# Performance work log

Measured on AMD Instinct MI355X. Metric: run time of the kernel, lower is better.

## Reference

```python
import jax, jax.numpy as jnp
import numpy as np

EPS = 1e-5

def conv3x3(x, w, b, stride=1):
    y = jax.lax.conv_general_dilated(x, w, (stride, stride), ((1, 1), (1, 1)),
                                     dimension_numbers=('NCHW', 'OIHW', 'NCHW'))
    return y + b[None, :, None, None]

def batchnorm(x, gamma, beta):
    # training-mode BN (PyTorch default): biased batch statistics over N,H,W
    mean = x.mean((0, 2, 3), keepdims=True)
    var = ((x - mean) ** 2).mean((0, 2, 3), keepdims=True)
    return (x - mean) * jax.lax.rsqrt(var + EPS) * gamma[None, :, None, None] + beta[None, :, None, None]

def deform_conv3x3(x, offset, w, b):
    # torchvision DeformConv2d: kernel 3x3, stride 1, pad 1, deform_groups=1
    B, C, H, W = x.shape
    K = 3
    off = offset.reshape(B, K * K, 2, H, W)  # per kernel tap: (dy, dx)
    ky, kx = jnp.meshgrid(jnp.arange(K) - 1, jnp.arange(K) - 1, indexing='ij')
    ky = ky.reshape(-1).astype(x.dtype)  # [9]
    kx = kx.reshape(-1).astype(x.dtype)
    y0 = jnp.arange(H, dtype=x.dtype)[:, None]
    x0 = jnp.arange(W, dtype=x.dtype)[None, :]
    py = y0[None, None] + ky[None, :, None, None] + off[:, :, 0]  # [B,9,H,W]
    px = x0[None, None] + kx[None, :, None, None] + off[:, :, 1]
    y_lo = jnp.floor(py)
    x_lo = jnp.floor(px)
    ly = (py - y_lo)[:, None]  # [B,1,9,H,W]
    lx = (px - x_lo)[:, None]
    xf = x.reshape(B, C, H * W)

    def gather(iy, ix):
        valid = ((iy >= 0) & (iy < H) & (ix >= 0) & (ix < W)).astype(x.dtype)
        iyc = jnp.clip(iy, 0, H - 1).astype(jnp.int32)
        ixc = jnp.clip(ix, 0, W - 1).astype(jnp.int32)
        idx = iyc * W + ixc  # [B,9,H,W]
        g = jax.vmap(lambda xb, ib: xb[:, ib.reshape(-1)].reshape(C, K * K, H, W))(xf, idx)
        return g * valid[:, None]  # zero padding outside -> [B,C,9,H,W]

    v00 = gather(y_lo, x_lo)
    v01 = gather(y_lo, x_lo + 1)
    v10 = gather(y_lo + 1, x_lo)
    v11 = gather(y_lo + 1, x_lo + 1)
    sampled = (v00 * (1 - ly) * (1 - lx) + v01 * (1 - ly) * lx
               + v10 * ly * (1 - lx) + v11 * ly * lx)  # [B,C,9,H,W]
    out = jnp.einsum('bckhw,ock->bohw', sampled, w.reshape(w.shape[0], C, K * K))
    return out + b[None, :, None, None]


def setup_inputs() -> dict:
    key = jax.random.key(0)
    ks = jax.random.split(key, 8)
    B, C, H, W = 4, 128, 64, 64
    x = jax.random.normal(ks[0], (B, C, H, W), jnp.float32)
    w_off = jax.random.normal(ks[1], (18, C, 3, 3), jnp.float32) * 0.01  # small offsets
    b_off = jnp.zeros((18,), jnp.float32)
    w_d = jax.random.normal(ks[2], (C, C, 3, 3), jnp.float32) * 0.03
    b_d = jnp.zeros((C,), jnp.float32)
    w1 = jax.random.normal(ks[3], (C, C, 3, 3), jnp.float32) * 0.03
    b1 = jnp.zeros((C,), jnp.float32)
    g1 = jnp.ones((C,), jnp.float32)
    beta1 = jnp.zeros((C,), jnp.float32)
    w2 = jax.random.normal(ks[4], (C, C, 3, 3), jnp.float32) * 0.03
    b2 = jnp.zeros((C,), jnp.float32)
    g2 = jnp.ones((C,), jnp.float32)
    beta2 = jnp.zeros((C,), jnp.float32)
    return {"x": x, "w_off": w_off, "b_off": b_off, "w_d": w_d, "b_d": b_d,
            "w1": w1, "b1": b1, "g1": g1, "beta1": beta1,
            "w2": w2, "b2": b2, "g2": g2, "beta2": beta2}


def reference(x, w_off, b_off, w_d, b_d, w1, b1, g1, beta1, w2, b2, g2, beta2):
    offset = conv3x3(x, w_off, b_off)
    d_out = deform_conv3x3(x, offset, w_d, b_d)
    out = jax.nn.relu(batchnorm(conv3x3(x, w1, b1), g1, beta1))
    out = batchnorm(conv3x3(out, w2, b2), g2, beta2)
    return jax.nn.relu(d_out + out)
```

## Files before the change

kernel.cpp:

```cpp
#include <hip/hip_runtime.h>

#define HH 64
#define WW 64
#define CC 128
#define HWSZ 4096

typedef __attribute__((ext_vector_type(8))) short short8v;
typedef __attribute__((ext_vector_type(4))) short short4v;
typedef __attribute__((ext_vector_type(4))) float floatx4;

__device__ __forceinline__ unsigned short f2bf(float f) {
    unsigned u = __float_as_uint(f);
    return (unsigned short)((u + 0x7FFFu + ((u >> 16) & 1u)) >> 16);
}
__device__ __forceinline__ float bf2f(unsigned short h) {
    return __uint_as_float(((unsigned)h) << 16);
}

__global__ void prepack_k(const float* __restrict__ w, unsigned short* __restrict__ blob,
                          int oc_total, int OCP)
{
    int i = blockIdx.x * 256 + threadIdx.x;
    if (i >= 36 * OCP * 32) return;
    int kr = i & 31;
    int rest = i >> 5;
    int oc = rest % OCP;
    int kc = rest / OCP;
    int k = kc * 32 + kr;
    float v = 0.f;
    if (oc < oc_total) v = w[((size_t)oc * CC + k / 9) * 9 + (k % 9)];
    unsigned short h = f2bf(v);
    unsigned short l = f2bf(v - bf2f(h));
    size_t base = (size_t)(kc * 2) * OCP * 40;
    blob[base + (size_t)oc * 40 + kr] = h;
    blob[base + (size_t)(OCP + oc) * 40 + kr] = l;
}

template<int TAG, int OCP, int MFR, int NFR, int WM, bool BN_IN, bool STATS>
__global__ __launch_bounds__(256)
void gemm_k(const float* __restrict__ in, const float* __restrict__ blobf,
            const float* __restrict__ bias,
            const float* __restrict__ bnscale, const float* __restrict__ bnshift,
            float* __restrict__ out, float* __restrict__ ssum, float* __restrict__ ssq,
            int oc_total)
{
    __shared__ __align__(16) unsigned short Al[2][64][40];
    __shared__ __align__(16) unsigned short Bl[2][OCP][40];
    const int tid = threadIdx.x;
    const int lane = tid & 63;
    const int wid = tid >> 6;
    const int b = blockIdx.x >> 6;
    const int y = blockIdx.x & 63;
    const int wm = wid % WM;
    const int wn = wid / WM;
    const int m0 = wm * MFR * 16;
    const int n0 = wn * NFR * 16;
    const int lrow = lane & 15;
    const int lkg  = (lane >> 4) * 8;

    floatx4 acc[MFR][NFR];
#pragma unroll
    for (int mi = 0; mi < MFR; ++mi)
#pragma unroll
        for (int nj = 0; nj < NFR; ++nj)
            acc[mi][nj] = {0.f, 0.f, 0.f, 0.f};

    const unsigned short* blb = (const unsigned short*)blobf;
    const float* inb = in + (size_t)b * CC * HWSZ;
    const int px = tid & 63;
    const int kr0 = (tid >> 6) * 8;

    for (int kc = 0; kc < 36; ++kc) {
        __syncthreads();
        short8v vh, vl;
#pragma unroll
        for (int j = 0; j < 8; ++j) {
            int k = kc * 32 + kr0 + j;
            int ic = k / 9;
            int kk = k - ic * 9;
            int ky = kk / 3;
            int gy = y + ky - 1;
            int gx = px + (kk - ky * 3) - 1;
            float v = 0.f;
            if ((unsigned)gy < (unsigned)HH && (unsigned)gx < (unsigned)WW) {
                v = inb[(size_t)ic * HWSZ + gy * WW + gx];
                if (BN_IN) v = fmaxf(fmaf(v, bnscale[ic], bnshift[ic]), 0.f);
            }
            unsigned short h = f2bf(v);
            vh[j] = (short)h;
            vl[j] = (short)f2bf(v - bf2f(h));
        }
        *(short8v*)&Al[0][px][kr0] = vh;
        *(short8v*)&Al[1][px][kr0] = vl;
        {
            const float4* src = (const float4*)(blb + (size_t)(kc * 2) * OCP * 40);
            float4* dst = (float4*)&Bl[0][0][0];
            const int n16 = (2 * OCP * 40) / 8;
            for (int i = tid; i < n16; i += 256) dst[i] = src[i];
        }
        __syncthreads();
        short8v af[2][MFR], bfr[2][NFR];
#pragma unroll
        for (int mi = 0; mi < MFR; ++mi) {
            af[0][mi] = *(const short8v*)&Al[0][m0 + mi * 16 + lrow][lkg];
            af[1][mi] = *(const short8v*)&Al[1][m0 + mi * 16 + lrow][lkg];
        }
#pragma unroll
        for (int nj = 0; nj < NFR; ++nj) {
            bfr[0][nj] = *(const short8v*)&Bl[0][n0 + nj * 16 + lrow][lkg];
            bfr[1][nj] = *(const short8v*)&Bl[1][n0 + nj * 16 + lrow][lkg];
        }
#pragma unroll
        for (int mi = 0; mi < MFR; ++mi)
#pragma unroll
            for (int nj = 0; nj < NFR; ++nj) {
                acc[mi][nj] = __builtin_amdgcn_mfma_f32_16x16x32_bf16(af[0][mi], bfr[0][nj], acc[mi][nj], 0, 0, 0);
                acc[mi][nj] = __builtin_amdgcn_mfma_f32_16x16x32_bf16(af[0][mi], bfr[1][nj], acc[mi][nj], 0, 0, 0);
                acc[mi][nj] = __builtin_amdgcn_mfma_f32_16x16x32_bf16(af[1][mi], bfr[0][nj], acc[mi][nj], 0, 0, 0);
            }
    }
#pragma unroll
    for (int nj = 0; nj < NFR; ++nj) {
        int oc = n0 + nj * 16 + lrow;
        float bv = (oc < oc_total) ? bias[oc] : 0.f;
        float s = 0.f, q = 0.f;
#pragma unroll
        for (int mi = 0; mi < MFR; ++mi) {
            floatx4 r = acc[mi][nj];
            r.x += bv; r.y += bv; r.z += bv; r.w += bv;
            if (oc < oc_total) {
                int pxq = m0 + mi * 16 + (lane >> 4) * 4;
                *(float4*)(out + ((size_t)b * oc_total + oc) * HWSZ + y * WW + pxq) =
                    make_float4(r.x, r.y, r.z, r.w);
            }
            if (STATS) {
                s += r.x + r.y + r.z + r.w;
                q += r.x * r.x + r.y * r.y + r.z * r.z + r.w * r.w;
            }
        }
        if (STATS) {
            s += __shfl_xor(s, 16); q += __shfl_xor(q, 16);
            s += __shfl_xor(s, 32); q += __shfl_xor(q, 32);
            if (lane < 16) { atomicAdd(&ssum[oc], s); atomicAdd(&ssq[oc], q); }
        }
    }
}

__global__ __launch_bounds__(512)
void dgemm_k(const float* __restrict__ x, const float* __restrict__ off,
             const float* __restrict__ blobf, const float* __restrict__ bd,
             float* __restrict__ dout)
{
    __shared__ __align__(16) unsigned short Al[2][64][40];
    __shared__ __align__(16) unsigned short Bl[2][CC][40];
    __shared__ __align__(16) float tw[9][64][4];
    __shared__ __align__(16) int   ti[9][64][4];
    const int tid = threadIdx.x;
    const int lane = tid & 63;
    const int wid = tid >> 6;
    const int b = blockIdx.x >> 6;
    const int y = blockIdx.x & 63;
    const int wm = wid & 1;
    const int wn = wid >> 1;
    const int m0 = wm * 32;
    const int n0 = wn * 32;
    const int lrow = lane & 15;
    const int lkg  = (lane >> 4) * 8;

    for (int e = tid; e < 9 * 64; e += 512) {
        int kk = e >> 6, px = e & 63;
        const float* ob = off + (size_t)b * 18 * HWSZ + y * WW + px;
        float dyv = ob[(2 * kk + 0) * HWSZ];
        float dxv = ob[(2 * kk + 1) * HWSZ];
        float fy = (float)(y + kk / 3 - 1) + dyv;
        float fx = (float)(px + kk % 3 - 1) + dxv;
        float yl = floorf(fy), xl = floorf(fx);
        float ly = fy - yl, lx = fx - xl;
        int iy0 = (int)yl, ix0 = (int)xl;
        int iy1 = iy0 + 1, ix1 = ix0 + 1;
        float vy0 = (iy0 >= 0 && iy0 < HH) ? 1.f : 0.f;
        float vy1 = (iy1 >= 0 && iy1 < HH) ? 1.f : 0.f;
        float vx0 = (ix0 >= 0 && ix0 < WW) ? 1.f : 0.f;
        float vx1 = (ix1 >= 0 && ix1 < WW) ? 1.f : 0.f;
        int iy0c = min(max(iy0, 0), HH - 1), iy1c = min(max(iy1, 0), HH - 1);
        int ix0c = min(max(ix0, 0), WW - 1), ix1c = min(max(ix1, 0), WW - 1);
        ti[kk][px][0] = iy0c * WW + ix0c;
        ti[kk][px][1] = iy0c * WW + ix1c;
        ti[kk][px][2] = iy1c * WW + ix0c;
        ti[kk][px][3] = iy1c * WW + ix1c;
        tw[kk][px][0] = (1.f - ly) * (1.f - lx) * vy0 * vx0;
        tw[kk][px][1] = (1.f - ly) * lx         * vy0 * vx1;
        tw[kk][px][2] = ly * (1.f - lx) * vy1 * vx0;
        tw[kk][px][3] = ly * lx         * vy1 * vx1;
    }

    floatx4 acc[2][2];
#pragma unroll
    for (int mi = 0; mi < 2; ++mi)
#pragma unroll
        for (int nj = 0; nj < 2; ++nj)
            acc[mi][nj] = {0.f, 0.f, 0.f, 0.f};

    const unsigned short* blb = (const unsigned short*)blobf;
    const float* xb = x + (size_t)b * CC * HWSZ;
    const int px = tid & 63;
    const int kr0 = (tid >> 6) * 4;

    for (int kc = 0; kc < 36; ++kc) {
        __syncthreads();
        short4v vh, vl;
#pragma unroll
        for (int j = 0; j < 4; ++j) {
            int k = kc * 32 + kr0 + j;
            int ic = k / 9;
            int kk = k - ic * 9;
            const float* xc = xb + (size_t)ic * HWSZ;
            float4 w4 = *(const float4*)&tw[kk][px][0];
            int4   i4 = *(const int4*)&ti[kk][px][0];
            float v =      w4.x * xc[i4.x];
            v = fmaf(w4.y, xc[i4.y], v);
            v = fmaf(w4.z, xc[i4.z], v);
            v = fmaf(w4.w, xc[i4.w], v);
            unsigned short h = f2bf(v);
            vh[j] = (short)h;
            vl[j] = (short)f2bf(v - bf2f(h));
        }
        *(short4v*)&Al[0][px][kr0] = vh;
        *(short4v*)&Al[1][px][kr0] = vl;
        {
            const float4* src = (const float4*)(blb + (size_t)(kc * 2) * CC * 40);
            float4* dst = (float4*)&Bl[0][0][0];
            const int n16 = (2 * CC * 40) / 8;
            for (int i = tid; i < n16; i += 512) dst[i] = src[i];
        }
        __syncthreads();
        short8v af[2][2], bfr[2][2];
#pragma unroll
        for (int mi = 0; mi < 2; ++mi) {
            af[0][mi] = *(const short8v*)&Al[0][m0 + mi * 16 + lrow][lkg];
            af[1][mi] = *(const short8v*)&Al[1][m0 + mi * 16 + lrow][lkg];
        }
#pragma unroll
        for (int nj = 0; nj < 2; ++nj) {
            bfr[0][nj] = *(const short8v*)&Bl[0][n0 + nj * 16 + lrow][lkg];
            bfr[1][nj] = *(const short8v*)&Bl[1][n0 + nj * 16 + lrow][lkg];
        }
#pragma unroll
        for (int mi = 0; mi < 2; ++mi)
#pragma unroll
            for (int nj = 0; nj < 2; ++nj) {
                acc[mi][nj] = __builtin_amdgcn_mfma_f32_16x16x32_bf16(af[0][mi], bfr[0][nj], acc[mi][nj], 0, 0, 0);
                acc[mi][nj] = __builtin_amdgcn_mfma_f32_16x16x32_bf16(af[0][mi], bfr[1][nj], acc[mi][nj], 0, 0, 0);
                acc[mi][nj] = __builtin_amdgcn_mfma_f32_16x16x32_bf16(af[1][mi], bfr[0][nj], acc[mi][nj], 0, 0, 0);
            }
    }
#pragma unroll
    for (int nj = 0; nj < 2; ++nj) {
        int oc = n0 + nj * 16 + lrow;
        float bv = bd[oc];
#pragma unroll
        for (int mi = 0; mi < 2; ++mi) {
            floatx4 r = acc[mi][nj];
            int pxq = m0 + mi * 16 + (lane >> 4) * 4;
            *(float4*)(dout + ((size_t)b * CC + oc) * HWSZ + y * WW + pxq) =
                make_float4(r.x + bv, r.y + bv, r.z + bv, r.w + bv);
        }
    }
}

__global__ void bnstat_k(const float* __restrict__ ssum, const float* __restrict__ ssq,
                         const float* __restrict__ g, const float* __restrict__ bet,
                         float* __restrict__ scale, float* __restrict__ shift)
{
    int c = threadIdx.x;
    const float invn = 1.f / (4.f * HWSZ);
    float mean = ssum[c] * invn;
    float var  = ssq[c] * invn - mean * mean;
    float sc = g[c] * rsqrtf(var + 1e-5f);
    scale[c] = sc;
    shift[c] = fmaf(-mean, sc, bet[c]);
}

__global__ __launch_bounds__(256)
void final_k(const float* __restrict__ dout, const float* __restrict__ y2,
             const float* __restrict__ scale, const float* __restrict__ shift,
             float* __restrict__ out)
{
    int i = blockIdx.x * 256 + threadIdx.x;
    int c = (i >> 10) & 127;
    float4 d = reinterpret_cast<const float4*>(dout)[i];
    float4 yv = reinterpret_cast<const float4*>(y2)[i];
    float sc = scale[c], sh = shift[c];
    float4 r;
    r.x = fmaxf(d.x + fmaf(yv.x, sc, sh), 0.f);
    r.y = fmaxf(d.y + fmaf(yv.y, sc, sh), 0.f);
    r.z = fmaxf(d.z + fmaf(yv.z, sc, sh), 0.f);
    r.w = fmaxf(d.w + fmaf(yv.w, sc, sh), 0.f);
    reinterpret_cast<float4*>(out)[i] = r;
}

extern "C" void kernel_launch(void* const* d_in, const int* in_sizes, int n_in,
                              void* d_out, int out_size, void* d_ws, size_t ws_size,
                              hipStream_t stream)
{
    const float* x     = (const float*)d_in[0];
    const float* w_off = (const float*)d_in[1];
    const float* b_off = (const float*)d_in[2];
    const float* w_d   = (const float*)d_in[3];
    const float* b_d   = (const float*)d_in[4];
    const float* w1    = (const float*)d_in[5];
    const float* b1    = (const float*)d_in[6];
    const float* g1    = (const float*)d_in[7];
    const float* be1   = (const float*)d_in[8];
    const float* w2    = (const float*)d_in[9];
    const float* b2    = (const float*)d_in[10];
    const float* g2    = (const float*)d_in[11];
    const float* be2   = (const float*)d_in[12];

    float* ws      = (float*)d_ws;
    float* off_buf = ws;
    float* y1      = off_buf + 294912;
    float* y2      = y1 + 2097152;
    float* dob     = y2 + 2097152;
    float* wo_blob = dob + 2097152;
    float* w1_blob = wo_blob + 46080;
    float* w2_blob = w1_blob + 184320;
    float* wd_blob = w2_blob + 184320;
    float* st      = wd_blob + 184320;

    hipMemsetAsync(st, 0, 512 * sizeof(float), stream);

    prepack_k<<<(36 * 32 * 32 + 255) / 256, 256, 0, stream>>>(w_off, (unsigned short*)wo_blob, 18, 32);
    prepack_k<<<(36 * 128 * 32 + 255) / 256, 256, 0, stream>>>(w1, (unsigned short*)w1_blob, 128, 128);
    prepack_k<<<(36 * 128 * 32 + 255) / 256, 256, 0, stream>>>(w2, (unsigned short*)w2_blob, 128, 128);
    prepack_k<<<(36 * 128 * 32 + 255) / 256, 256, 0, stream>>>(w_d, (unsigned short*)wd_blob, 128, 128);

    gemm_k<0, 32, 1, 2, 4, false, false><<<256, 256, 0, stream>>>(
        x, wo_blob, b_off, nullptr, nullptr, off_buf, nullptr, nullptr, 18);

    dgemm_k<<<256, 512, 0, stream>>>(x, off_buf, wd_blob, b_d, dob);

    gemm_k<1, 128, 2, 4, 2, false, true><<<256, 256, 0, stream>>>(
        x, w1_blob, b1, nullptr, nullptr, y1, st, st + 128, 128);
    bnstat_k<<<1, 128, 0, stream>>>(st, st + 128, g1, be1, st + 512, st + 640);

    gemm_k<2, 128, 2, 4, 2, true, true><<<256, 256, 0, stream>>>(
        y1, w2_blob, b2, st + 512, st + 640, y2, st + 256, st + 384, 128);
    bnstat_k<<<1, 128, 0, stream>>>(st + 256, st + 384, g2, be2, st + 768, st + 896);

    final_k<<<dim3(2048), 256, 0, stream>>>(dob, y2, st + 768, st + 896, (float*)d_out);
}
```

Baseline: 453.4 us.

## Double-buffer LDS tiles with register prefetch in conv GEMMs; use 512 threads

The conv GEMM kernels and the deformable GEMM now use two LDS buffers. The next K-chunk's global loads (input gather and weight blob) are issued into registers before the MFMAs on the current chunk, then written to the other buffer afterwards. This removes one barrier per iteration and is meant to hide global-load latency behind the matrix math. The two 128-channel conv GEMMs also move from 256 to 512 threads per block with smaller per-wave tiles. The costs are doubled LDS use and extra prefetch registers, which may lower occupancy.

```diff
diff --git a/kernel.cpp b/kernel.cpp
--- a/kernel.cpp
+++ b/kernel.cpp
@@ -36,16 +36,19 @@
     blob[base + (size_t)(OCP + oc) * 40 + kr] = l;
 }
 
-template<int TAG, int OCP, int MFR, int NFR, int WM, bool BN_IN, bool STATS>
-__global__ __launch_bounds__(256)
+template<int TAG, int OCP, int THREADS, int WM, int MFR, int NFR, bool BN_IN, bool STATS>
+__global__ __launch_bounds__(THREADS)
 void gemm_k(const float* __restrict__ in, const float* __restrict__ blobf,
             const float* __restrict__ bias,
             const float* __restrict__ bnscale, const float* __restrict__ bnshift,
             float* __restrict__ out, float* __restrict__ ssum, float* __restrict__ ssq,
             int oc_total)
 {
-    __shared__ __align__(16) unsigned short Al[2][64][40];
-    __shared__ __align__(16) unsigned short Bl[2][OCP][40];
+    constexpr int KPT   = 2048 / THREADS;
+    constexpr int NB4   = OCP * 10;
+    constexpr int NITER = (NB4 + THREADS - 1) / THREADS;
+    __shared__ __align__(16) unsigned short Al[2][2][64][40];
+    __shared__ __align__(16) unsigned short Bl[2][2][OCP][40];
     const int tid = threadIdx.x;
     const int lane = tid & 63;
     const int wid = tid >> 6;
@@ -68,47 +71,83 @@
     const unsigned short* blb = (const unsigned short*)blobf;
     const float* inb = in + (size_t)b * CC * HWSZ;
     const int px = tid & 63;
-    const int kr0 = (tid >> 6) * 8;
-
-    for (int kc = 0; kc < 36; ++kc) {
-        __syncthreads();
-        short8v vh, vl;
-#pragma unroll
-        for (int j = 0; j < 8; ++j) {
+    const int kr0 = (tid >> 6) * KPT;
+
+    float  aval[KPT], asc[KPT], ash[KPT];
+    float4 breg[NITER];
+
+    auto load_stage = [&](int kc) {
+#pragma unroll
+        for (int j = 0; j < KPT; ++j) {
             int k = kc * 32 + kr0 + j;
             int ic = k / 9;
             int kk = k - ic * 9;
             int ky = kk / 3;
             int gy = y + ky - 1;
             int gx = px + (kk - ky * 3) - 1;
-            float v = 0.f;
-            if ((unsigned)gy < (unsigned)HH && (unsigned)gx < (unsigned)WW) {
-                v = inb[(size_t)ic * HWSZ + gy * WW + gx];
-                if (BN_IN) v = fmaxf(fmaf(v, bnscale[ic], bnshift[ic]), 0.f);
-            }
-            unsigned short h = f2bf(v);
-            vh[j] = (short)h;
-            vl[j] = (short)f2bf(v - bf2f(h));
-        }
-        *(short8v*)&Al[0][px][kr0] = vh;
-        *(short8v*)&Al[1][px][kr0] = vl;
-        {
-            const float4* src = (const float4*)(blb + (size_t)(kc * 2) * OCP * 40);
-            float4* dst = (float4*)&Bl[0][0][0];
-            const int n16 = (2 * OCP * 40) / 8;
-            for (int i = tid; i < n16; i += 256) dst[i] = src[i];
-        }
-        __syncthreads();
+            aval[j] = ((unsigned)gy < (unsigned)HH && (unsigned)gx < (unsigned)WW)
+                      ? inb[(size_t)ic * HWSZ + gy * WW + gx] : 0.f;
+            if (BN_IN) { asc[j] = bnscale[ic]; ash[j] = bnshift[ic]; }
+        }
+        const float4* src = (const float4*)(blb + (size_t)(kc * 2) * OCP * 40);
+#pragma unroll
+        for (int t = 0; t < NITER; ++t) {
+            int idx = tid + t * THREADS;
+            if (idx < NB4) breg[t] = src[idx];
+        }
+    };
+    auto write_stage = [&](int buf) {
+        if constexpr (KPT == 4) {
+            short4v vh, vl;
+#pragma unroll
+            for (int j = 0; j < 4; ++j) {
+                float v = aval[j];
+                if (BN_IN) v = fmaxf(fmaf(v, asc[j], ash[j]), 0.f);
+                unsigned short h = f2bf(v);
+                vh[j] = (short)h;
+                vl[j] = (short)f2bf(v - bf2f(h));
+            }
+            *(short4v*)&Al[buf][0][px][kr0] = vh;
+            *(short4v*)&Al[buf][1][px][kr0] = vl;
+        } else {
+            short8v vh, vl;
+#pragma unroll
+            for (int j = 0; j < 8; ++j) {
+                float v = aval[j];
+                if (BN_IN) v = fmaxf(fmaf(v, asc[j], ash[j]), 0.f);
+                unsigned short h = f2bf(v);
+                vh[j] = (short)h;
+                vl[j] = (short)f2bf(v - bf2f(h));
+            }
+            *(short8v*)&Al[buf][0][px][kr0] = vh;
+            *(short8v*)&Al[buf][1][px][kr0] = vl;
+        }
+        float4* dst = (float4*)&Bl[buf][0][0][0];
+#pragma unroll
+        for (int t = 0; t < NITER; ++t) {
+            int idx = tid + t * THREADS;
+            if (idx < NB4) dst[idx] = breg[t];
+        }
+    };
+
+    load_stage(0);
+    write_stage(0);
+    __syncthreads();
+
+    for (int kc = 0; kc < 36; ++kc) {
+        const int cur = kc & 1;
+        if (kc < 35) load_stage(kc + 1);
+
         short8v af[2][MFR], bfr[2][NFR];
 #pragma unroll
         for (int mi = 0; mi < MFR; ++mi) {
-            af[0][mi] = *(const short8v*)&Al[0][m0 + mi * 16 + lrow][lkg];
-            af[1][mi] = *(const short8v*)&Al[1][m0 + mi * 16 + lrow][lkg];
+            af[0][mi] = *(const short8v*)&Al[cur][0][m0 + mi * 16 + lrow][lkg];
+            af[1][mi] = *(const short8v*)&Al[cur][1][m0 + mi * 16 + lrow][lkg];
         }
 #pragma unroll
         for (int nj = 0; nj < NFR; ++nj) {
-            bfr[0][nj] = *(const short8v*)&Bl[0][n0 + nj * 16 + lrow][lkg];
-            bfr[1][nj] = *(const short8v*)&Bl[1][n0 + nj * 16 + lrow][lkg];
+            bfr[0][nj] = *(const short8v*)&Bl[cur][0][n0 + nj * 16 + lrow][lkg];
+            bfr[1][nj] = *(const short8v*)&Bl[cur][1][n0 + nj * 16 + lrow][lkg];
         }
 #pragma unroll
         for (int mi = 0; mi < MFR; ++mi)
@@ -118,7 +157,11 @@
                 acc[mi][nj] = __builtin_amdgcn_mfma_f32_16x16x32_bf16(af[0][mi], bfr[1][nj], acc[mi][nj], 0, 0, 0);
                 acc[mi][nj] = __builtin_amdgcn_mfma_f32_16x16x32_bf16(af[1][mi], bfr[0][nj], acc[mi][nj], 0, 0, 0);
             }
+
+        if (kc < 35) write_stage(cur ^ 1);
+        __syncthreads();
     }
+
 #pragma unroll
     for (int nj = 0; nj < NFR; ++nj) {
         int oc = n0 + nj * 16 + lrow;
@@ -151,8 +194,9 @@
              const float* __restrict__ blobf, const float* __restrict__ bd,
              float* __restrict__ dout)
 {
-    __shared__ __align__(16) unsigned short Al[2][64][40];
-    __shared__ __align__(16) unsigned short Bl[2][CC][40];
+    constexpr int NITER = 3;
+    __shared__ __align__(16) unsigned short Al[2][2][64][40];
+    __shared__ __align__(16) unsigned short Bl[2][2][CC][40];
     __shared__ __align__(16) float tw[9][64][4];
     __shared__ __align__(16) int   ti[9][64][4];
     const int tid = threadIdx.x;
@@ -206,44 +250,74 @@
     const int px = tid & 63;
     const int kr0 = (tid >> 6) * 4;
 
-    for (int kc = 0; kc < 36; ++kc) {
-        __syncthreads();
-        short4v vh, vl;
+    float  g4[4][4];
+    float4 breg[NITER];
+
+    auto load_stage = [&](int kc) {
 #pragma unroll
         for (int j = 0; j < 4; ++j) {
             int k = kc * 32 + kr0 + j;
             int ic = k / 9;
             int kk = k - ic * 9;
             const float* xc = xb + (size_t)ic * HWSZ;
+            int4 i4 = *(const int4*)&ti[kk][px][0];
+            g4[j][0] = xc[i4.x];
+            g4[j][1] = xc[i4.y];
+            g4[j][2] = xc[i4.z];
+            g4[j][3] = xc[i4.w];
+        }
+        const float4* src = (const float4*)(blb + (size_t)(kc * 2) * CC * 40);
+#pragma unroll
+        for (int t = 0; t < NITER; ++t) {
+            int idx = tid + t * 512;
+            if (idx < CC * 10) breg[t] = src[idx];
+        }
+    };
+    auto write_stage = [&](int buf, int kc) {
+        short4v vh, vl;
+#pragma unroll
+        for (int j = 0; j < 4; ++j) {
+            int k = kc * 32 + kr0 + j;
+            int ic = k / 9;
+            int kk = k - ic * 9;
             float4 w4 = *(const float4*)&tw[kk][px][0];
-            int4   i4 = *(const int4*)&ti[kk][px][0];
-            float v =      w4.x * xc[i4.x];
-            v = fmaf(w4.y, xc[i4.y], v);
-            v = fmaf(w4.z, xc[i4.z], v);
-            v = fmaf(w4.w, xc[i4.w], v);
+            float v =      w4.x * g4[j][0];
+            v = fmaf(w4.y, g4[j][1], v);
+            v = fmaf(w4.z, g4[j][2], v);
+            v = fmaf(w4.w, g4[j][3], v);
             unsigned short h = f2bf(v);
             vh[j] = (short)h;
             vl[j] = (short)f2bf(v - bf2f(h));
         }
-        *(short4v*)&Al[0][px][kr0] = vh;
-        *(short4v*)&Al[1][px][kr0] = vl;
-        {
-            const float4* src = (const float4*)(blb + (size_t)(kc * 2) * CC * 40);
-            float4* dst = (float4*)&Bl[0][0][0];
-            const int n16 = (2 * CC * 40) / 8;
-            for (int i = tid; i < n16; i += 512) dst[i] = src[i];
-        }
-        __syncthreads();
+        *(short4v*)&Al[buf][0][px][kr0] = vh;
+        *(short4v*)&Al[buf][1][px][kr0] = vl;
+        float4* dst = (float4*)&Bl[buf][0][0][0];
+#pragma unroll
+        for (int t = 0; t < NITER; ++t) {
+            int idx = tid + t * 512;
+            if (idx < CC * 10) dst[idx] = breg[t];
+        }
+    };
+
+    __syncthreads();
+    load_stage(0);
+    write_stage(0, 0);
+    __syncthreads();
+
+    for (int kc = 0; kc < 36; ++kc) {
+        const int cur = kc & 1;
+        if (kc < 35) load_stage(kc + 1);
+
         short8v af[2][2], bfr[2][2];
 #pragma unroll
         for (int mi = 0; mi < 2; ++mi) {
-            af[0][mi] = *(const short8v*)&Al[0][m0 + mi * 16 + lrow][lkg];
-            af[1][mi] = *(const short8v*)&Al[1][m0 + mi * 16 + lrow][lkg];
+            af[0][mi] = *(const short8v*)&Al[cur][0][m0 + mi * 16 + lrow][lkg];
+            af[1][mi] = *(const short8v*)&Al[cur][1][m0 + mi * 16 + lrow][lkg];
         }
 #pragma unroll
         for (int nj = 0; nj < 2; ++nj) {
-            bfr[0][nj] = *(const short8v*)&Bl[0][n0 + nj * 16 + lrow][lkg];
-            bfr[1][nj] = *(const short8v*)&Bl[1][n0 + nj * 16 + lrow][lkg];
+            bfr[0][nj] = *(const short8v*)&Bl[cur][0][n0 + nj * 16 + lrow][lkg];
+            bfr[1][nj] = *(const short8v*)&Bl[cur][1][n0 + nj * 16 + lrow][lkg];
         }
 #pragma unroll
         for (int mi = 0; mi < 2; ++mi)
@@ -253,7 +327,11 @@
                 acc[mi][nj] = __builtin_amdgcn_mfma_f32_16x16x32_bf16(af[0][mi], bfr[1][nj], acc[mi][nj], 0, 0, 0);
                 acc[mi][nj] = __builtin_amdgcn_mfma_f32_16x16x32_bf16(af[1][mi], bfr[0][nj], acc[mi][nj], 0, 0, 0);
             }
+
+        if (kc < 35) write_stage(cur ^ 1, kc + 1);
+        __syncthreads();
     }
+
 #pragma unroll
     for (int nj = 0; nj < 2; ++nj) {
         int oc = n0 + nj * 16 + lrow;
@@ -335,16 +413,16 @@
     prepack_k<<<(36 * 128 * 32 + 255) / 256, 256, 0, stream>>>(w2, (unsigned short*)w2_blob, 128, 128);
     prepack_k<<<(36 * 128 * 32 + 255) / 256, 256, 0, stream>>>(w_d, (unsigned short*)wd_blob, 128, 128);
 
-    gemm_k<0, 32, 1, 2, 4, false, false><<<256, 256, 0, stream>>>(
+    gemm_k<0, 32, 256, 4, 1, 2, false, false><<<256, 256, 0, stream>>>(
         x, wo_blob, b_off, nullptr, nullptr, off_buf, nullptr, nullptr, 18);
 
     dgemm_k<<<256, 512, 0, stream>>>(x, off_buf, wd_blob, b_d, dob);
 
-    gemm_k<1, 128, 2, 4, 2, false, true><<<256, 256, 0, stream>>>(
+    gemm_k<1, 128, 512, 2, 2, 2, false, true><<<256, 512, 0, stream>>>(
         x, w1_blob, b1, nullptr, nullptr, y1, st, st + 128, 128);
     bnstat_k<<<1, 128, 0, stream>>>(st, st + 128, g1, be1, st + 512, st + 640);
 
-    gemm_k<2, 128, 2, 4, 2, true, true><<<256, 256, 0, stream>>>(
+    gemm_k<2, 128, 512, 2, 2, 2, true, true><<<256, 512, 0, stream>>>(
         y1, w2_blob, b2, st + 512, st + 640, y2, st + 256, st + 384, 128);
     bnstat_k<<<1, 128, 0, stream>>>(st + 256, st + 384, g2, be2, st + 768, st + 896);
 
```

Result: faster. 434.9 us (-4.1%).
